# Kernel optimization log

Measured on AMD Instinct MI355X. Metric: run time of the kernel, lower is better.

## Reference

```python
import jax, jax.numpy as jnp
import numpy as np
import math

B, S, DIM = 2, 2048, 4096
N_HEADS, N_KV_HEADS = 32, 8
HEAD_DIM = DIM // N_HEADS  # 128
N_REP = N_HEADS // N_KV_HEADS  # 4
ROPE_THETA = 10000.0


def setup_inputs() -> dict:
    key = jax.random.key(0)
    ks = jax.random.split(key, 6)
    x = jax.random.normal(ks[0], (B, S, DIM), dtype=jnp.float32)
    wq = jax.random.normal(ks[1], (DIM, DIM), dtype=jnp.float32) * 0.02
    wk = jax.random.normal(ks[2], (N_KV_HEADS * HEAD_DIM, DIM), dtype=jnp.float32) * 0.02
    wv = jax.random.normal(ks[3], (N_KV_HEADS * HEAD_DIM, DIM), dtype=jnp.float32) * 0.02
    wo = jax.random.normal(ks[4], (DIM, DIM), dtype=jnp.float32) * 0.02
    # rotary freqs_cis (seqlen, head_dim//2), represented as cos/sin
    inv_freq = 1.0 / (ROPE_THETA ** (jnp.arange(0, HEAD_DIM, 2, dtype=jnp.float32) / HEAD_DIM))
    angles = jnp.arange(S, dtype=jnp.float32)[:, None] * inv_freq[None, :]  # [S, HEAD_DIM//2]
    freqs_cos = jnp.cos(angles)
    freqs_sin = jnp.sin(angles)
    # additive causal mask [S, S]: 0 on/below diagonal, -inf above
    mask = jnp.where(jnp.tril(jnp.ones((S, S), dtype=bool)), 0.0, -jnp.inf).astype(jnp.float32)
    return {"x": x, "wq": wq, "wk": wk, "wv": wv, "wo": wo,
            "freqs_cos": freqs_cos, "freqs_sin": freqs_sin, "mask": mask}


def _apply_rotary(t, freqs_cos, freqs_sin):
    # t: [B, S, H, HEAD_DIM]; interpret pairs (even, odd) as complex
    t2 = t.reshape(*t.shape[:-1], HEAD_DIM // 2, 2)
    tr, ti = t2[..., 0], t2[..., 1]
    c = freqs_cos[None, :, None, :]  # [1, S, 1, HD/2]
    s = freqs_sin[None, :, None, :]
    out_r = tr * c - ti * s
    out_i = tr * s + ti * c
    return jnp.stack([out_r, out_i], axis=-1).reshape(t.shape)


def reference(x, wq, wk, wv, wo, freqs_cos, freqs_sin, mask):
    bsz, seqlen, _ = x.shape
    xq = (x @ wq.T).reshape(bsz, seqlen, N_HEADS, HEAD_DIM)
    xk = (x @ wk.T).reshape(bsz, seqlen, N_KV_HEADS, HEAD_DIM)
    xv = (x @ wv.T).reshape(bsz, seqlen, N_KV_HEADS, HEAD_DIM)
    xq = _apply_rotary(xq, freqs_cos, freqs_sin)
    xk = _apply_rotary(xk, freqs_cos, freqs_sin)
    # repeat_kv (GQA): [B,S,KV,HD] -> [B,S,KV*N_REP,HD] via repeat_interleave on head axis
    keys = jnp.repeat(xk, N_REP, axis=2)
    values = jnp.repeat(xv, N_REP, axis=2)
    # scores: [B, H, S, S]
    scores = jnp.einsum('bqhd,bkhd->bhqk', xq, keys) / math.sqrt(HEAD_DIM)
    scores = scores + mask[None, None, :, :]
    probs = jax.nn.softmax(scores.astype(jnp.float32), axis=-1).astype(xq.dtype)
    out = jnp.einsum('bhqk,bkhd->bqhd', probs, values).reshape(bsz, seqlen, DIM)
    return out @ wo.T
```

## Files before the change

kernel.cpp:

```cpp
#include <hip/hip_runtime.h>

typedef __bf16 bf16;
typedef __bf16 bf16x4 __attribute__((ext_vector_type(4)));
typedef __bf16 bf16x8 __attribute__((ext_vector_type(8)));
typedef float f32x4 __attribute__((ext_vector_type(4)));

#define BB 2
#define SS 2048
#define DIM 4096
#define KVDIM 1024
#define NH 32
#define NKV 8
#define HD 128
#define NEGINF (-1e30f)

__device__ __forceinline__ void async16(void* lds, const void* gmem) {
    __builtin_amdgcn_global_load_lds(
        (const __attribute__((address_space(1))) void*)gmem,
        (__attribute__((address_space(3))) void*)lds, 16, 0, 0);
}

__device__ __forceinline__ f32x4 mfma16(bf16x8 a, bf16x8 b, f32x4 c) {
    return __builtin_amdgcn_mfma_f32_16x16x32_bf16(a, b, c, 0, 0, 0);
}

struct DetectArgs { const void* p[7]; int n[7]; };

__global__ void detect_dtypes(DetectArgs a, int* flags) {
    __shared__ int bad;
    const int ti = blockIdx.x;
    if (threadIdx.x == 0) bad = 0;
    __syncthreads();
    const bf16* s = (const bf16*)a.p[ti];
    int n = a.n[ti];
    int take = n < 8192 ? n : 8192;
    int lbad = 0;
    for (int i = threadIdx.x; i < take; i += 256) {
        float f = (float)s[i];
        if (!(f > -1e4f && f < 1e4f)) lbad = 1;
    }
    if (lbad) atomicOr(&bad, 1);
    __syncthreads();
    if (threadIdx.x == 0) flags[ti] = bad;
}

__global__ void convert_to_bf16(const void* __restrict__ src, bf16* __restrict__ dst,
                                int n8, const int* __restrict__ flagp) {
    int i = blockIdx.x * 256 + threadIdx.x;
    if (i >= n8) return;
    if (*flagp) {
        const float* s = (const float*)src + (size_t)i * 8;
        bf16x8 v;
#pragma unroll
        for (int j = 0; j < 8; ++j) v[j] = (bf16)s[j];
        *(bf16x8*)(dst + (size_t)i * 8) = v;
    } else {
        *(bf16x8*)(dst + (size_t)i * 8) = *((const bf16x8*)src + i);
    }
}

#define SBAR()  asm volatile("s_barrier" ::: "memory")
#define LGKM0() asm volatile("s_waitcnt lgkmcnt(0)" ::: "memory")
#define VM4()   asm volatile("s_waitcnt vmcnt(4)" ::: "memory")

__device__ __forceinline__ void gemm256_core(const bf16* __restrict__ A,
                                             const bf16* __restrict__ B,
                                             int K, int m0, int n0,
                                             f32x4 (&acc)[8][4]) {
    __shared__ bf16 sm[2][4][8192];
    const int t = threadIdx.x;
    const int lane = t & 63;
    const int w = t >> 6;
    const int l15 = lane & 15, quad = lane >> 4;
    const int wm = w >> 2;
    const int wn = w & 3;
    const int axr = l15 & 7;
    const int c0 = (quad ^ axr) * 8;
    const int c1 = ((4 + quad) ^ axr) * 8;
    const int srl = t >> 3;
    const int sch = ((t & 7) ^ (srl & 7)) * 8;
    const size_t Ks = (size_t)K;

    bf16x8 aReg[4][2], bReg[4][2];

#define RD_A(c_, mh) { \
    const bf16* ab = &sm[c_][wm][0] + ((mh) * 64 + l15) * 64; \
    _Pragma("unroll") for (int i = 0; i < 4; ++i) { \
        aReg[i][0] = *(const bf16x8*)(ab + i * 1024 + c0); \
        aReg[i][1] = *(const bf16x8*)(ab + i * 1024 + c1); } }

#define RD_B(c_, nh) { \
    const bf16* bb = &sm[c_][2 + (wn >> 1)][0] + ((wn & 1) * 64 + (nh) * 32 + l15) * 64; \
    _Pragma("unroll") for (int jj = 0; jj < 2; ++jj) { \
        bReg[(nh) * 2 + jj][0] = *(const bf16x8*)(bb + jj * 1024 + c0); \
        bReg[(nh) * 2 + jj][1] = *(const bf16x8*)(bb + jj * 1024 + c1); } }

#define STG(c_, reg_, Mat, rowbase, kt) { \
    bf16* d_ = &sm[c_][reg_][0] + (size_t)t * 8; \
    const bf16* s_ = (Mat) + ((size_t)((rowbase) + srl)) * Ks + (size_t)(kt) * 64 + sch; \
    async16(d_, s_); \
    async16(d_ + 4096, s_ + 64 * Ks); }

#define MM(mh, nh) { \
    _Pragma("unroll") for (int i = 0; i < 4; ++i) \
    _Pragma("unroll") for (int jj = 0; jj < 2; ++jj) { \
        acc[(mh) * 4 + i][(nh) * 2 + jj] = \
            mfma16(aReg[i][0], bReg[(nh) * 2 + jj][0], acc[(mh) * 4 + i][(nh) * 2 + jj]); \
        acc[(mh) * 4 + i][(nh) * 2 + jj] = \
            mfma16(aReg[i][1], bReg[(nh) * 2 + jj][1], acc[(mh) * 4 + i][(nh) * 2 + jj]); } }

    STG(0, 0, A, m0, 0);
    STG(0, 2, B, n0, 0);
    STG(0, 1, A, m0 + 128, 0);
    STG(0, 3, B, n0 + 128, 0);
    STG(1, 2, B, n0, 1);
    STG(1, 0, A, m0, 1);
    VM4(); SBAR();

    const int NT = K >> 6;
    for (int T = 0; T < NT; ++T) {
        const int c = T & 1, nc = c ^ 1;
        const int kt1 = (T + 1 < NT) ? T + 1 : 0;
        const int kt2 = (T + 2 < NT) ? T + 2 : 0;
        RD_A(c, 0); RD_B(c, 0);
        STG(nc, 1, A, m0 + 128, kt1);
        SBAR();
        __builtin_amdgcn_s_setprio(1); MM(0, 0); __builtin_amdgcn_s_setprio(0);
        LGKM0(); SBAR();
        RD_B(c, 1);
        STG(nc, 3, B, n0 + 128, kt1);
        SBAR();
        __builtin_amdgcn_s_setprio(1); MM(0, 1); __builtin_amdgcn_s_setprio(0);
        LGKM0(); SBAR();
        RD_A(c, 1);
        STG(c, 2, B, n0, kt2);
        SBAR();
        __builtin_amdgcn_s_setprio(1); MM(1, 0); __builtin_amdgcn_s_setprio(0);
        LGKM0(); SBAR();
        STG(c, 0, A, m0, kt2);
        SBAR();
        __builtin_amdgcn_s_setprio(1); MM(1, 1); __builtin_amdgcn_s_setprio(0);
        LGKM0(); VM4(); SBAR();
    }
#undef RD_A
#undef RD_B
#undef STG
#undef MM
}

__global__ __launch_bounds__(512, 2)
void gemm_nt(const bf16* __restrict__ A, const bf16* __restrict__ B,
             bf16* __restrict__ C, int M, int N, int K) {
    const int t = threadIdx.x, lane = t & 63, w = t >> 6;
    const int l15 = lane & 15, quad = lane >> 4;
    const int wm = w >> 2, wn = w & 3;
    const int m0 = blockIdx.y * 256, n0 = blockIdx.x * 256;
    f32x4 acc[8][4] = {};
    gemm256_core(A, B, K, m0, n0, acc);
#pragma unroll
    for (int i = 0; i < 8; ++i)
#pragma unroll
        for (int j = 0; j < 4; ++j) {
            int col = n0 + wn * 64 + j * 16 + l15;
#pragma unroll
            for (int r = 0; r < 4; ++r)
                C[(size_t)(m0 + wm * 128 + i * 16 + quad * 4 + r) * N + col] = (bf16)acc[i][j][r];
        }
}

__global__ __launch_bounds__(512, 2)
void gemm_nt_kv(const bf16* __restrict__ A, const bf16* __restrict__ Bkv,
                bf16* __restrict__ Kc, bf16* __restrict__ Vc, int M, int K) {
    const int t = threadIdx.x, lane = t & 63, w = t >> 6;
    const int l15 = lane & 15, quad = lane >> 4;
    const int wm = w >> 2, wn = w & 3;
    const int m0 = blockIdx.y * 256, n0 = blockIdx.x * 256;
    f32x4 acc[8][4] = {};
    gemm256_core(A, Bkv, K, m0, n0, acc);
    bf16* C = (n0 < KVDIM) ? Kc : Vc;
    const int cb = (n0 < KVDIM) ? n0 : n0 - KVDIM;
#pragma unroll
    for (int i = 0; i < 8; ++i)
#pragma unroll
        for (int j = 0; j < 4; ++j) {
            int col = cb + wn * 64 + j * 16 + l15;
#pragma unroll
            for (int r = 0; r < 4; ++r)
                C[(size_t)(m0 + wm * 128 + i * 16 + quad * 4 + r) * KVDIM + col] = (bf16)acc[i][j][r];
        }
}

__global__ __launch_bounds__(512, 2)
void gemm_nt_out(const bf16* __restrict__ A, const bf16* __restrict__ B,
                 void* __restrict__ C, int M, int N, int K,
                 const int* __restrict__ flagp) {
    const int t = threadIdx.x, lane = t & 63, w = t >> 6;
    const int l15 = lane & 15, quad = lane >> 4;
    const int wm = w >> 2, wn = w & 3;
    const int m0 = blockIdx.y * 256, n0 = blockIdx.x * 256;
    const int f32out = *flagp;
    f32x4 acc[8][4] = {};
    gemm256_core(A, B, K, m0, n0, acc);
#pragma unroll
    for (int i = 0; i < 8; ++i)
#pragma unroll
        for (int j = 0; j < 4; ++j) {
            int col = n0 + wn * 64 + j * 16 + l15;
#pragma unroll
            for (int r = 0; r < 4; ++r) {
                int row = m0 + wm * 128 + i * 16 + quad * 4 + r;
                if (f32out) ((float*)C)[(size_t)row * N + col] = acc[i][j][r];
                else        ((bf16*)C)[(size_t)row * N + col] = (bf16)acc[i][j][r];
            }
        }
}

__device__ __forceinline__ void rope8(bf16* p, const bf16* fc, const bf16* fs,
                                      int s, int i0, float sc) {
    bf16x8 v = *(bf16x8*)p;
    bf16x8 o;
#pragma unroll
    for (int j = 0; j < 4; ++j) {
        float tr = (float)v[2 * j], ti = (float)v[2 * j + 1];
        float cc = (float)fc[s * 64 + i0 + j];
        float sn = (float)fs[s * 64 + i0 + j];
        o[2 * j]     = (bf16)((tr * cc - ti * sn) * sc);
        o[2 * j + 1] = (bf16)((tr * sn + ti * cc) * sc);
    }
    *(bf16x8*)p = o;
}

__global__ void rope_kernel(bf16* __restrict__ Q, bf16* __restrict__ Kr,
                            const bf16* __restrict__ fc, const bf16* __restrict__ fs) {
    const float qscale = 0.08838834764831845f * 1.4426950408889634f;
    int u = blockIdx.x * 256 + threadIdx.x;
    const int QU = (DIM * (BB * SS)) / 8;
    if (u < QU) {
        int row = u >> 9;
        int c = (u & 511) * 8;
        rope8(Q + (size_t)row * DIM + c, fc, fs, row & (SS - 1), (c >> 1) & 63, qscale);
    } else {
        u -= QU;
        int row = u >> 7;
        int c = (u & 127) * 8;
        rope8(Kr + (size_t)row * KVDIM + c, fc, fs, row & (SS - 1), (c >> 1) & 63, 1.0f);
    }
}

__global__ void transpose_v(const bf16* __restrict__ V, bf16* __restrict__ Vt) {
    __shared__ bf16 tile[64][74];
    const int st = blockIdx.x, ct = blockIdx.y, b = blockIdx.z;
    const int s0 = st * 64;
    const int kvh = ct >> 1, d0 = (ct & 1) * 64;
    const int t = threadIdx.x;
#pragma unroll
    for (int i = 0; i < 2; ++i) {
        int o = i * 256 + t;
        int r = o >> 3, c8 = (o & 7) * 8;
        bf16x8 v = *(const bf16x8*)(V + (size_t)(b * SS + s0 + r) * KVDIM + kvh * HD + d0 + c8);
#pragma unroll
        for (int j = 0; j < 8; ++j) tile[r][c8 + j] = v[j];
    }
    __syncthreads();
#pragma unroll
    for (int i = 0; i < 2; ++i) {
        int o = i * 256 + t;
        int sseg = (o & 7) * 8, dl = o >> 3;
        bf16x8 v;
#pragma unroll
        for (int j = 0; j < 8; ++j) v[j] = tile[sseg + j][dl];
        *(bf16x8*)(Vt + ((size_t)((b * NKV + kvh) * HD) + d0 + dl) * SS + s0 + sseg) = v;
    }
}

__global__ __launch_bounds__(256, 2)
void flash_attn(const bf16* __restrict__ Q, const bf16* __restrict__ Kr,
                const bf16* __restrict__ Vt, bf16* __restrict__ AO) {
    __shared__ char smem[51200];
    bf16* Ks  = (bf16*)smem;
    bf16* Vts = (bf16*)(smem + 16384);
    bf16* Ps2 = (bf16*)(smem + 32768);
    const int t = threadIdx.x, w = t >> 6, lane = t & 63;
    const int l15 = lane & 15, quad = lane >> 4;
    const int bh = blockIdx.x;
    const int b = bh >> 5, h = bh & 31, kvh = h >> 2;
    const int q0 = ((int)gridDim.y - 1 - (int)blockIdx.y) * 128;

    bf16x8 qf[2][4];
#pragma unroll
    for (int mi = 0; mi < 2; ++mi) {
        int qrow = b * SS + q0 + w * 32 + mi * 16 + l15;
#pragma unroll
        for (int ks = 0; ks < 4; ++ks)
            qf[mi][ks] = *(const bf16x8*)(Q + (size_t)qrow * DIM + h * HD + ks * 32 + quad * 8);
    }

    f32x4 of[2][8] = {};
    float mrow[2] = {NEGINF, NEGINF};
    float lrow[2] = {0.f, 0.f};

    const int kend = q0 + 128;
    for (int kk = 0; kk < kend; kk += 64) {
#pragma unroll
        for (int i = 0; i < 4; ++i) {
            int s = i * 256 + t;
            int key = s >> 4, slot = s & 15;
            int dseg = slot ^ (key & 15);
            async16((char*)Ks + (size_t)s * 16,
                    Kr + (size_t)(b * SS + kk + key) * KVDIM + kvh * HD + dseg * 8);
        }
#pragma unroll
        for (int i = 0; i < 4; ++i) {
            int s = i * 256 + t;
            int d = s >> 3, slot = s & 7;
            int kseg = slot ^ (d & 7);
            async16((char*)Vts + (size_t)s * 16,
                    Vt + ((size_t)((b * NKV + kvh) * HD + d)) * SS + kk + kseg * 8);
        }
        __syncthreads();

        f32x4 sacc[2][4] = {};
#pragma unroll
        for (int nt = 0; nt < 4; ++nt) {
            int key = nt * 16 + l15;
#pragma unroll
            for (int ks = 0; ks < 4; ++ks) {
                int slot = (ks * 4 + quad) ^ (key & 15);
                bf16x8 kf = *(const bf16x8*)(Ks + key * 128 + slot * 8);
#pragma unroll
                for (int mi = 0; mi < 2; ++mi)
                    sacc[mi][nt] = mfma16(kf, qf[mi][ks], sacc[mi][nt]);
            }
        }
        if (kk >= q0) {
#pragma unroll
            for (int mi = 0; mi < 2; ++mi) {
                int q = q0 + w * 32 + mi * 16 + l15;
#pragma unroll
                for (int nt = 0; nt < 4; ++nt) {
                    int kbase = kk + nt * 16 + quad * 4;
#pragma unroll
                    for (int r = 0; r < 4; ++r)
                        if (kbase + r > q) sacc[mi][nt][r] = NEGINF;
                }
            }
        }
#pragma unroll
        for (int mi = 0; mi < 2; ++mi) {
            float mx = sacc[mi][0][0];
#pragma unroll
            for (int nt = 0; nt < 4; ++nt)
#pragma unroll
                for (int r = 0; r < 4; ++r) mx = fmaxf(mx, sacc[mi][nt][r]);
            mx = fmaxf(mx, __shfl_xor(mx, 16));
            mx = fmaxf(mx, __shfl_xor(mx, 32));
            float mnew = fmaxf(mrow[mi], mx);
            float alpha = exp2f(mrow[mi] - mnew);
            float rsum = 0.f;
#pragma unroll
            for (int nt = 0; nt < 4; ++nt)
#pragma unroll
                for (int r = 0; r < 4; ++r) {
                    float p = exp2f(sacc[mi][nt][r] - mnew);
                    sacc[mi][nt][r] = p;
                    rsum += p;
                }
            rsum += __shfl_xor(rsum, 16);
            rsum += __shfl_xor(rsum, 32);
            lrow[mi] = lrow[mi] * alpha + rsum;
            mrow[mi] = mnew;
#pragma unroll
            for (int dt = 0; dt < 8; ++dt)
#pragma unroll
                for (int r = 0; r < 4; ++r) of[mi][dt][r] *= alpha;
        }
#pragma unroll
        for (int mi = 0; mi < 2; ++mi) {
            int row = w * 32 + mi * 16 + l15;
#pragma unroll
            for (int nt = 0; nt < 4; ++nt) {
                bf16x4 pv;
#pragma unroll
                for (int r = 0; r < 4; ++r) pv[r] = (bf16)sacc[mi][nt][r];
                *(bf16x4*)(Ps2 + row * 72 + nt * 16 + quad * 4) = pv;
            }
        }
#pragma unroll
        for (int kb = 0; kb < 2; ++kb) {
            bf16x8 pa[2];
#pragma unroll
            for (int mi = 0; mi < 2; ++mi)
                pa[mi] = *(const bf16x8*)(Ps2 + (w * 32 + mi * 16 + l15) * 72 + kb * 32 + quad * 8);
#pragma unroll
            for (int dt = 0; dt < 8; ++dt) {
                int d = dt * 16 + l15;
                int slot = (kb * 4 + quad) ^ (d & 7);
                bf16x8 vb = *(const bf16x8*)(Vts + d * 64 + slot * 8);
#pragma unroll
                for (int mi = 0; mi < 2; ++mi)
                    of[mi][dt] = mfma16(vb, pa[mi], of[mi][dt]);
            }
        }
        __syncthreads();
    }
    bf16* Os = (bf16*)smem;
#pragma unroll
    for (int mi = 0; mi < 2; ++mi) {
        float inv = 1.0f / lrow[mi];
        int row = w * 32 + mi * 16 + l15;
#pragma unroll
        for (int dt = 0; dt < 8; ++dt) {
            bf16x4 o4;
#pragma unroll
            for (int r = 0; r < 4; ++r) o4[r] = (bf16)(of[mi][dt][r] * inv);
            int s = dt * 2 + (quad >> 1);
            int slot = s ^ l15;
            *(bf16x4*)((char*)Os + row * 256 + slot * 16 + (quad & 1) * 8) = o4;
        }
    }
    __syncthreads();
#pragma unroll
    for (int i = 0; i < 8; ++i) {
        int flat = i * 256 + t;
        int ql = flat >> 4, s = flat & 15;
        bf16x8 v = *(const bf16x8*)((char*)Os + ql * 256 + (s ^ (ql & 15)) * 16);
        *(bf16x8*)(AO + (size_t)(b * SS + q0 + ql) * DIM + h * HD + s * 8) = v;
    }
}

extern "C" void kernel_launch(void* const* d_in, const int* in_sizes, int n_in,
                              void* d_out, int out_size, void* d_ws, size_t ws_size,
                              hipStream_t stream) {
    const size_t MD = (size_t)BB * SS * DIM;
    const size_t KV = (size_t)BB * SS * KVDIM;
    const size_t FC = (size_t)SS * (HD / 2);
    const int M = BB * SS;

    int* flags = (int*)d_ws;
    bf16* xb  = (bf16*)((char*)d_ws + 32);
    bf16* wb  = xb + MD;
    bf16* Q   = wb + MD;
    bf16* Kr  = Q + MD;
    bf16* Vw  = Kr + KV;
    bf16* Vt  = Vw + KV;
    bf16* fcb = Vt + KV;
    bf16* fsb = fcb + FC;

    DetectArgs da;
    for (int i = 0; i < 7; ++i) { da.p[i] = d_in[i]; da.n[i] = in_sizes[i]; }
    detect_dtypes<<<7, 256, 0, stream>>>(da, flags);

    dim3 blk(256);
    dim3 blk512(512);
    convert_to_bf16<<<(int)(MD / 8 / 256), blk, 0, stream>>>(d_in[0], xb, (int)(MD / 8), flags + 0);
    convert_to_bf16<<<(int)(FC / 8 / 256), blk, 0, stream>>>(d_in[5], fcb, (int)(FC / 8), flags + 5);
    convert_to_bf16<<<(int)(FC / 8 / 256), blk, 0, stream>>>(d_in[6], fsb, (int)(FC / 8), flags + 6);

    convert_to_bf16<<<(int)(MD / 8 / 256), blk, 0, stream>>>(d_in[1], wb, (int)(MD / 8), flags + 1);
    gemm_nt<<<dim3(DIM / 256, M / 256), blk512, 0, stream>>>(xb, wb, Q, M, DIM, DIM);

    convert_to_bf16<<<(int)(KV / 8 / 256), blk, 0, stream>>>(d_in[2], wb, (int)(KV / 8), flags + 2);
    convert_to_bf16<<<(int)(KV / 8 / 256), blk, 0, stream>>>(d_in[3], wb + KV, (int)(KV / 8), flags + 3);
    gemm_nt_kv<<<dim3(2 * KVDIM / 256, M / 256), blk512, 0, stream>>>(xb, wb, Kr, Vw, M, DIM);

    rope_kernel<<<dim3((int)((MD / 8 + KV / 8) / 256)), blk, 0, stream>>>(Q, Kr, fcb, fsb);
    transpose_v<<<dim3(SS / 64, 16, BB), blk, 0, stream>>>(Vw, Vt);

    flash_attn<<<dim3(BB * NH, SS / 128), blk, 0, stream>>>(Q, Kr, Vt, xb);

    convert_to_bf16<<<(int)(MD / 8 / 256), blk, 0, stream>>>(d_in[4], wb, (int)(MD / 8), flags + 4);
    gemm_nt_out<<<dim3(DIM / 256, M / 256), blk512, 0, stream>>>(xb, wb, d_out, M, DIM, DIM, flags + 0);
}
```

Before: 735.3 us.

## Shrink flash-attention LDS, overlap V loads with softmax, and skip rescales

The flash attention kernel now puts the P tile in the K buffer region, cutting shared memory to 32KB, and raises launch bounds to 4 blocks per CU. It waits only for the K loads before computing scores, so the V loads overlap QK^T and softmax, with a full vmcnt wait and barrier before P is written. A wave-uniform lazy rescale skips the alpha rescaling of the output accumulator when the new row max grows by no more than 8 (log2 units). Tighter register limits may cause spills, and the lazy rescale relies on fp32 headroom.

```diff
diff --git a/kernel.cpp b/kernel.cpp
--- a/kernel.cpp
+++ b/kernel.cpp
@@ -62,6 +62,7 @@
 #define SBAR()  asm volatile("s_barrier" ::: "memory")
 #define LGKM0() asm volatile("s_waitcnt lgkmcnt(0)" ::: "memory")
 #define VM4()   asm volatile("s_waitcnt vmcnt(4)" ::: "memory")
+#define VM0()   asm volatile("s_waitcnt vmcnt(0)" ::: "memory")
 
 __device__ __forceinline__ void gemm256_core(const bf16* __restrict__ A,
                                              const bf16* __restrict__ B,
@@ -273,13 +274,13 @@
     }
 }
 
-__global__ __launch_bounds__(256, 2)
+__global__ __launch_bounds__(256, 4)
 void flash_attn(const bf16* __restrict__ Q, const bf16* __restrict__ Kr,
                 const bf16* __restrict__ Vt, bf16* __restrict__ AO) {
-    __shared__ char smem[51200];
+    __shared__ char smem[32768];
     bf16* Ks  = (bf16*)smem;
     bf16* Vts = (bf16*)(smem + 16384);
-    bf16* Ps2 = (bf16*)(smem + 32768);
+    char* Ps  = smem;
     const int t = threadIdx.x, w = t >> 6, lane = t & 63;
     const int l15 = lane & 15, quad = lane >> 4;
     const int bh = blockIdx.x;
@@ -317,7 +318,7 @@
             async16((char*)Vts + (size_t)s * 16,
                     Vt + ((size_t)((b * NKV + kvh) * HD + d)) * SS + kk + kseg * 8);
         }
-        __syncthreads();
+        VM4(); SBAR();
 
         f32x4 sacc[2][4] = {};
 #pragma unroll
@@ -347,33 +348,56 @@
         }
 #pragma unroll
         for (int mi = 0; mi < 2; ++mi) {
-            float mx = sacc[mi][0][0];
+            float m01[4];
 #pragma unroll
             for (int nt = 0; nt < 4; ++nt)
-#pragma unroll
-                for (int r = 0; r < 4; ++r) mx = fmaxf(mx, sacc[mi][nt][r]);
+                m01[nt] = fmaxf(fmaxf(sacc[mi][nt][0], sacc[mi][nt][1]),
+                                fmaxf(sacc[mi][nt][2], sacc[mi][nt][3]));
+            float mx = fmaxf(fmaxf(m01[0], m01[1]), fmaxf(m01[2], m01[3]));
             mx = fmaxf(mx, __shfl_xor(mx, 16));
             mx = fmaxf(mx, __shfl_xor(mx, 32));
-            float mnew = fmaxf(mrow[mi], mx);
-            float alpha = exp2f(mrow[mi] - mnew);
-            float rsum = 0.f;
-#pragma unroll
-            for (int nt = 0; nt < 4; ++nt)
-#pragma unroll
-                for (int r = 0; r < 4; ++r) {
-                    float p = exp2f(sacc[mi][nt][r] - mnew);
-                    sacc[mi][nt][r] = p;
-                    rsum += p;
+            if (__all(mx - mrow[mi] <= 8.0f)) {
+                float rs[4];
+#pragma unroll
+                for (int nt = 0; nt < 4; ++nt) {
+                    rs[nt] = 0.f;
+#pragma unroll
+                    for (int r = 0; r < 4; ++r) {
+                        float p = exp2f(sacc[mi][nt][r] - mrow[mi]);
+                        sacc[mi][nt][r] = p;
+                        rs[nt] += p;
+                    }
                 }
-            rsum += __shfl_xor(rsum, 16);
-            rsum += __shfl_xor(rsum, 32);
-            lrow[mi] = lrow[mi] * alpha + rsum;
-            mrow[mi] = mnew;
-#pragma unroll
-            for (int dt = 0; dt < 8; ++dt)
-#pragma unroll
-                for (int r = 0; r < 4; ++r) of[mi][dt][r] *= alpha;
-        }
+                float rsum = (rs[0] + rs[1]) + (rs[2] + rs[3]);
+                rsum += __shfl_xor(rsum, 16);
+                rsum += __shfl_xor(rsum, 32);
+                lrow[mi] += rsum;
+            } else {
+                float mnew = fmaxf(mrow[mi], mx);
+                float alpha = exp2f(mrow[mi] - mnew);
+                float rs[4];
+#pragma unroll
+                for (int nt = 0; nt < 4; ++nt) {
+                    rs[nt] = 0.f;
+#pragma unroll
+                    for (int r = 0; r < 4; ++r) {
+                        float p = exp2f(sacc[mi][nt][r] - mnew);
+                        sacc[mi][nt][r] = p;
+                        rs[nt] += p;
+                    }
+                }
+                float rsum = (rs[0] + rs[1]) + (rs[2] + rs[3]);
+                rsum += __shfl_xor(rsum, 16);
+                rsum += __shfl_xor(rsum, 32);
+                lrow[mi] = lrow[mi] * alpha + rsum;
+                mrow[mi] = mnew;
+#pragma unroll
+                for (int dt = 0; dt < 8; ++dt)
+#pragma unroll
+                    for (int r = 0; r < 4; ++r) of[mi][dt][r] *= alpha;
+            }
+        }
+        VM0(); SBAR();
 #pragma unroll
         for (int mi = 0; mi < 2; ++mi) {
             int row = w * 32 + mi * 16 + l15;
@@ -382,15 +406,18 @@
                 bf16x4 pv;
 #pragma unroll
                 for (int r = 0; r < 4; ++r) pv[r] = (bf16)sacc[mi][nt][r];
-                *(bf16x4*)(Ps2 + row * 72 + nt * 16 + quad * 4) = pv;
+                int cc = nt * 2 + (quad >> 1);
+                *(bf16x4*)(Ps + row * 128 + ((cc ^ (row & 7)) * 16 + (quad & 1) * 8)) = pv;
             }
         }
 #pragma unroll
         for (int kb = 0; kb < 2; ++kb) {
             bf16x8 pa[2];
 #pragma unroll
-            for (int mi = 0; mi < 2; ++mi)
-                pa[mi] = *(const bf16x8*)(Ps2 + (w * 32 + mi * 16 + l15) * 72 + kb * 32 + quad * 8);
+            for (int mi = 0; mi < 2; ++mi) {
+                int row = w * 32 + mi * 16 + l15;
+                pa[mi] = *(const bf16x8*)(Ps + row * 128 + (((kb * 4 + quad) ^ (row & 7)) * 16));
+            }
 #pragma unroll
             for (int dt = 0; dt < 8; ++dt) {
                 int d = dt * 16 + l15;
@@ -401,7 +428,7 @@
                     of[mi][dt] = mfma16(vb, pa[mi], of[mi][dt]);
             }
         }
-        __syncthreads();
+        SBAR();
     }
     bf16* Os = (bf16*)smem;
 #pragma unroll
```

After: 1.101 ms. +49.7%, slower.
